# Kernel tuning notes

Hardware: AMD Instinct MI355X
Metric: run time of the kernel (lower is better)

Reference implementation:

```python
import jax, jax.numpy as jnp
import numpy as np

REDUCE_RATIO = 0.9

def reference(x, starts):
    # x: [B, T, C] float; starts: [B] int, start of the cropped window per sample.
    B, T, C = x.shape
    L = int(np.ceil(REDUCE_RATIO * T))  # target_len (static)
    # np.interp query points: linspace(0, L, num=T) against xp = arange(L).
    q = jnp.linspace(0.0, float(L), T, dtype=x.dtype)          # [T]
    t = jnp.clip(q, 0.0, float(L - 1))                          # np.interp clamps to edges
    lo = jnp.clip(jnp.floor(t), 0.0, float(L - 2)).astype(jnp.int32)  # [T]
    w = (t - lo.astype(x.dtype))[None, :, None]                 # [1, T, 1] interp weight
    # Absolute gather indices into the original series: start + local index.
    idx_lo = starts[:, None].astype(jnp.int32) + lo[None, :]    # [B, T]
    v_lo = jnp.take_along_axis(x, idx_lo[:, :, None], axis=1)       # [B, T, C]
    v_hi = jnp.take_along_axis(x, (idx_lo + 1)[:, :, None], axis=1)  # [B, T, C]
    return v_lo * (1.0 - w) + v_hi * w

def setup_inputs() -> dict:
    key = jax.random.key(0)
    k1, k2 = jax.random.split(key)
    B, T, C = 64, 4096, 128
    L = int(np.ceil(REDUCE_RATIO * T))
    x = jax.random.normal(k1, (B, T, C), dtype=jnp.float32)
    starts = jax.random.randint(k2, (B,), 0, T - L, dtype=jnp.int32)
    return {"x": x, "starts": starts}
```

## Files before the change

### kernel.cpp

```cpp
#include <hip/hip_runtime.h>


constexpr int B_ = 64;
constexpr int T_ = 4096;
constexpr int C_ = 128;
constexpr int L_ = 3687;
constexpr int C4 = C_ / 4;

__global__ __launch_bounds__(256)
void WindowSlice_kernel(const float4* __restrict__ x,
                        const int*    __restrict__ starts,
                        float4*       __restrict__ out) {
    const int tid = blockIdx.x * 256 + threadIdx.x;
    const int row = tid >> 5;
    const int c4  = tid & 31;
    const int b   = row >> 12;
    const int i   = row & (T_ - 1);

    const double step = (double)L_ / (double)(T_ - 1);
    double t = (double)i * step;
    if (t > (double)(L_ - 1)) t = (double)(L_ - 1);
    int lo = (int)t;
    if (lo > L_ - 2) lo = L_ - 2;
    const float w = (float)(t - (double)lo);

    const int start = starts[b];
    const long long base = ((long long)b * T_ + start + lo) * C4 + c4;

    const float4 vlo = x[base];
    const float4 vhi = x[base + C4];

    float4 o;
    o.x = fmaf(w, vhi.x - vlo.x, vlo.x);
    o.y = fmaf(w, vhi.y - vlo.y, vlo.y);
    o.z = fmaf(w, vhi.z - vlo.z, vlo.z);
    o.w = fmaf(w, vhi.w - vlo.w, vlo.w);

    out[(long long)row * C4 + c4] = o;
}

extern "C" void kernel_launch(void* const* d_in, const int* in_sizes, int n_in,
                              void* d_out, int out_size, void* d_ws, size_t ws_size,
                              hipStream_t stream) {
    const float4* x      = (const float4*)d_in[0];
    const int*    starts = (const int*)d_in[1];
    float4*       out    = (float4*)d_out;

    const int total_f4 = B_ * T_ * C4;
    const int blocks   = total_f4 / 256;
    WindowSlice_kernel<<<blocks, 256, 0, stream>>>(x, starts, out);
}
```

Before: 226.3 us.

## Process two rows per thread with XCD-aware block swizzle and nontemporal stores

Each block now covers 16 output rows, so each thread computes two rows and issues four loads before any math. Block IDs are remapped so that consecutive blocks on the same XCD work on contiguous rows, which should improve L2 reuse of the overlapping lo/hi source rows. Outputs are written with nontemporal stores to keep the streaming writes from evicting inputs in cache. The grid is halved and launch bounds request higher occupancy.

New measurement: 230.7 us. About the same (+2.0%).

```diff
diff --git a/kernel.cpp b/kernel.cpp
--- a/kernel.cpp
+++ b/kernel.cpp
@@ -6,37 +6,67 @@
 constexpr int C_ = 128;
 constexpr int L_ = 3687;
 constexpr int C4 = C_ / 4;
+constexpr int ROWS_PER_BLOCK = 16;
+constexpr int NBLK = B_ * T_ / ROWS_PER_BLOCK;
+constexpr int BLOCKS_PER_B = T_ / ROWS_PER_BLOCK;
+constexpr int NXCD = 8;
 
-__global__ __launch_bounds__(256)
+typedef float f32x4 __attribute__((ext_vector_type(4)));
+
+__global__ __launch_bounds__(256, 8)
 void WindowSlice_kernel(const float4* __restrict__ x,
                         const int*    __restrict__ starts,
                         float4*       __restrict__ out) {
-    const int tid = blockIdx.x * 256 + threadIdx.x;
-    const int row = tid >> 5;
-    const int c4  = tid & 31;
-    const int b   = row >> 12;
-    const int i   = row & (T_ - 1);
+    const int bid = blockIdx.x;
+    const int swz = (bid & (NXCD - 1)) * (NBLK / NXCD) + (bid >> 3);
+
+    const int b  = swz >> 8;
+    const int i0 = (swz & (BLOCKS_PER_B - 1)) * ROWS_PER_BLOCK;
+    const int c4 = threadIdx.x & 31;
+    const int rr = threadIdx.x >> 5;
+
+    const int start = starts[b];
 
     const double step = (double)L_ / (double)(T_ - 1);
-    double t = (double)i * step;
-    if (t > (double)(L_ - 1)) t = (double)(L_ - 1);
-    int lo = (int)t;
-    if (lo > L_ - 2) lo = L_ - 2;
-    const float w = (float)(t - (double)lo);
 
-    const int start = starts[b];
-    const long long base = ((long long)b * T_ + start + lo) * C4 + c4;
+    const int i_a = i0 + rr;
+    const int i_b = i_a + 8;
 
-    const float4 vlo = x[base];
-    const float4 vhi = x[base + C4];
+    double ta = (double)i_a * step;
+    if (ta > (double)(L_ - 1)) ta = (double)(L_ - 1);
+    int lo_a = (int)ta;
+    if (lo_a > L_ - 2) lo_a = L_ - 2;
+    const float wa = (float)(ta - (double)lo_a);
 
-    float4 o;
-    o.x = fmaf(w, vhi.x - vlo.x, vlo.x);
-    o.y = fmaf(w, vhi.y - vlo.y, vlo.y);
-    o.z = fmaf(w, vhi.z - vlo.z, vlo.z);
-    o.w = fmaf(w, vhi.w - vlo.w, vlo.w);
+    double tb = (double)i_b * step;
+    if (tb > (double)(L_ - 1)) tb = (double)(L_ - 1);
+    int lo_b = (int)tb;
+    if (lo_b > L_ - 2) lo_b = L_ - 2;
+    const float wb = (float)(tb - (double)lo_b);
 
-    out[(long long)row * C4 + c4] = o;
+    const long long brow = (long long)b * T_;
+    const long long base_a = (brow + start + lo_a) * C4 + c4;
+    const long long base_b = (brow + start + lo_b) * C4 + c4;
+
+    const float4 vlo_a = x[base_a];
+    const float4 vhi_a = x[base_a + C4];
+    const float4 vlo_b = x[base_b];
+    const float4 vhi_b = x[base_b + C4];
+
+    f32x4 oa, ob;
+    oa.x = fmaf(wa, vhi_a.x - vlo_a.x, vlo_a.x);
+    oa.y = fmaf(wa, vhi_a.y - vlo_a.y, vlo_a.y);
+    oa.z = fmaf(wa, vhi_a.z - vlo_a.z, vlo_a.z);
+    oa.w = fmaf(wa, vhi_a.w - vlo_a.w, vlo_a.w);
+
+    ob.x = fmaf(wb, vhi_b.x - vlo_b.x, vlo_b.x);
+    ob.y = fmaf(wb, vhi_b.y - vlo_b.y, vlo_b.y);
+    ob.z = fmaf(wb, vhi_b.z - vlo_b.z, vlo_b.z);
+    ob.w = fmaf(wb, vhi_b.w - vlo_b.w, vlo_b.w);
+
+    f32x4* outv = (f32x4*)out;
+    __builtin_nontemporal_store(oa, &outv[(brow + i_a) * C4 + c4]);
+    __builtin_nontemporal_store(ob, &outv[(brow + i_b) * C4 + c4]);
 }
 
 extern "C" void kernel_launch(void* const* d_in, const int* in_sizes, int n_in,
@@ -46,7 +76,5 @@
     const int*    starts = (const int*)d_in[1];
     float4*       out    = (float4*)d_out;
 
-    const int total_f4 = B_ * T_ * C4;
-    const int blocks   = total_f4 / 256;
-    WindowSlice_kernel<<<blocks, 256, 0, stream>>>(x, starts, out);
+    WindowSlice_kernel<<<NBLK, 256, 0, stream>>>(x, starts, out);
 }
```

## Stage input rows in LDS via direct global-to-LDS loads with XCD swizzle

Applied to the files above, without the earlier changes.

Each block now handles 32 output rows of one sample. It first copies the 32 covering input rows into shared memory using global_load_lds, then does both interpolation taps from LDS instead of issuing two global loads per output. The block index is swizzled so that neighbouring tiles land on the same XCD, and outputs use nontemporal stores. This is meant to cut redundant global and L2 traffic from the overlapping lo/hi reads, but it adds a barrier and relies on the 32-row input window always covering lo+1.

Result: slower. 232.8 us (+2.9%).

```diff
diff --git a/kernel.cpp b/kernel.cpp
--- a/kernel.cpp
+++ b/kernel.cpp
@@ -6,37 +6,77 @@
 constexpr int C_ = 128;
 constexpr int L_ = 3687;
 constexpr int C4 = C_ / 4;
+constexpr int ROWS_OUT = 32;
+constexpr int ROWS_IN  = 32;
+constexpr int NBLK = B_ * T_ / ROWS_OUT;
+constexpr int BLOCKS_PER_B = T_ / ROWS_OUT;
+constexpr int NXCD = 8;
 
-__global__ __launch_bounds__(256)
+typedef float f32x4 __attribute__((ext_vector_type(4)));
+typedef __attribute__((address_space(3))) void       lds_void;
+typedef __attribute__((address_space(1))) const void glob_void;
+
+__global__ __launch_bounds__(256, 8)
 void WindowSlice_kernel(const float4* __restrict__ x,
                         const int*    __restrict__ starts,
                         float4*       __restrict__ out) {
-    const int tid = blockIdx.x * 256 + threadIdx.x;
-    const int row = tid >> 5;
-    const int c4  = tid & 31;
-    const int b   = row >> 12;
-    const int i   = row & (T_ - 1);
+    __shared__ float4 lds[ROWS_IN * C4];
 
-    const double step = (double)L_ / (double)(T_ - 1);
-    double t = (double)i * step;
-    if (t > (double)(L_ - 1)) t = (double)(L_ - 1);
-    int lo = (int)t;
-    if (lo > L_ - 2) lo = L_ - 2;
-    const float w = (float)(t - (double)lo);
+    const int bid = blockIdx.x;
+    const int swz = (bid & (NXCD - 1)) * (NBLK / NXCD) + (bid >> 3);
+
+    const int b  = swz >> 7;
+    const int i0 = (swz & (BLOCKS_PER_B - 1)) * ROWS_OUT;
 
     const int start = starts[b];
-    const long long base = ((long long)b * T_ + start + lo) * C4 + c4;
 
-    const float4 vlo = x[base];
-    const float4 vhi = x[base + C4];
+    const int m0 = (i0 * L_) / (T_ - 1);
 
-    float4 o;
-    o.x = fmaf(w, vhi.x - vlo.x, vlo.x);
-    o.y = fmaf(w, vhi.y - vlo.y, vlo.y);
-    o.z = fmaf(w, vhi.z - vlo.z, vlo.z);
-    o.w = fmaf(w, vhi.w - vlo.w, vlo.w);
+    const long long xrow0 = ((long long)b * T_ + start) * C4;
 
-    out[(long long)row * C4 + c4] = o;
+    #pragma unroll
+    for (int k = 0; k < 4; ++k) {
+        const int idx = k * 256 + threadIdx.x;
+        const int r   = idx >> 5;
+        const int c   = idx & 31;
+        int g = m0 + r;
+        if (g > L_ - 1) g = L_ - 1;
+        const float4* src = x + (xrow0 + (long long)g * C4 + c);
+        __builtin_amdgcn_global_load_lds((glob_void*)src,
+                                         (lds_void*)&lds[idx], 16, 0, 0);
+    }
+    __syncthreads();
+
+    const int c4 = threadIdx.x & 31;
+    const int r0 = threadIdx.x >> 5;
+    const double step = (double)L_ / (double)(T_ - 1);
+
+    f32x4* outv = (f32x4*)out;
+    const long long obase = ((long long)b * T_ + i0) * C4 + c4;
+
+    #pragma unroll
+    for (int q = 0; q < 4; ++q) {
+        const int r = r0 + q * 8;
+        const int i = i0 + r;
+
+        double t = (double)i * step;
+        if (t > (double)(L_ - 1)) t = (double)(L_ - 1);
+        int lo = (int)t;
+        if (lo > L_ - 2) lo = L_ - 2;
+        const float w = (float)(t - (double)lo);
+
+        const int ll = lo - m0;
+        const float4 vlo = lds[ll * C4 + c4];
+        const float4 vhi = lds[(ll + 1) * C4 + c4];
+
+        f32x4 o;
+        o.x = fmaf(w, vhi.x - vlo.x, vlo.x);
+        o.y = fmaf(w, vhi.y - vlo.y, vlo.y);
+        o.z = fmaf(w, vhi.z - vlo.z, vlo.z);
+        o.w = fmaf(w, vhi.w - vlo.w, vlo.w);
+
+        __builtin_nontemporal_store(o, &outv[obase + (long long)r * C4]);
+    }
 }
 
 extern "C" void kernel_launch(void* const* d_in, const int* in_sizes, int n_in,
@@ -46,7 +86,5 @@
     const int*    starts = (const int*)d_in[1];
     float4*       out    = (float4*)d_out;
 
-    const int total_f4 = B_ * T_ * C4;
-    const int blocks   = total_f4 / 256;
-    WindowSlice_kernel<<<blocks, 256, 0, stream>>>(x, starts, out);
+    WindowSlice_kernel<<<NBLK, 256, 0, stream>>>(x, starts, out);
 }
```
